# Optimization experiments

Measured on AMD Instinct MI355X. Metric: run time of the kernel, lower is better.

Reference implementation:

```python
import jax, jax.numpy as jnp
import numpy as np

H = 512       # hidden_dim == node_init_dim
N_MAX = 128   # max nodes (upper bound on ADD_NODE count)
L = 1024      # action sequence length (padded with -1)
NEG = -1e9    # mask value for invalid destination logits


def _gru(x, h, wih, whh, bih, bhh):
    # PyTorch nn.GRUCell math; gates packed as [r, z, n] along dim 0.
    gi = wih @ x + bih
    gh = whh @ h + bhh
    d = h.shape[0]
    r = jax.nn.sigmoid(gi[:d] + gh[:d])
    z = jax.nn.sigmoid(gi[d:2 * d] + gh[d:2 * d])
    n = jnp.tanh(gi[2 * d:] + r * gh[2 * d:])
    return (1.0 - z) * n + z * h


def _make_actions(rng):
    # Synthesize a grammatically valid DGMG teacher-forcing trace:
    # ADD_NODE=0, ADD_EDGE=1, CHOOSE_DEST=2, STOP_EDGE=3, STOP_NODE=4, pad=-1
    acts, ags = [], []
    cur = -1
    while len(acts) < L - 8 and cur < N_MAX - 1:
        acts.append(0); ags.append(0)
        cur += 1
        if cur > 0:
            for _ in range(int(rng.integers(1, 4))):
                if len(acts) >= L - 4:
                    break
                acts.append(1); ags.append(0)
                acts.append(2); ags.append(int(rng.integers(0, cur)))
            acts.append(3); ags.append(0)
    acts.append(4); ags.append(0)
    pad = L - len(acts)
    acts += [-1] * pad
    ags += [0] * pad
    return np.array(acts, np.int64), np.array(ags, np.int64)


def setup_inputs() -> dict:
    rng = np.random.default_rng(0)
    acts, ags = _make_actions(rng)
    key = jax.random.key(0)
    ks = jax.random.split(key, 12)
    s = 0.02
    p = lambda k, shape: jax.random.normal(k, shape, jnp.float32) * s
    return {
        "actions": jnp.asarray(acts),
        "args_seq": jnp.asarray(ags),
        "node_init": p(ks[0], (H,)),
        "w_nip": p(ks[1], (H, H)), "b_nip": jnp.zeros((H,), jnp.float32),
        "w_e1": p(ks[2], (H, 2 * H)), "b_e1": jnp.zeros((H,), jnp.float32),
        "w_e2": p(ks[3], (2, H)), "b_e2": jnp.zeros((2,), jnp.float32),
        "w_q": p(ks[4], (H, 2 * H)), "b_q": jnp.zeros((H,), jnp.float32),
        "w_k": p(ks[5], (H, H)), "b_k": jnp.zeros((H,), jnp.float32),
        "wih_n": p(ks[6], (3 * H, H)), "whh_n": p(ks[7], (3 * H, H)),
        "bih_n": jnp.zeros((3 * H,), jnp.float32), "bhh_n": jnp.zeros((3 * H,), jnp.float32),
        "wih_g": p(ks[8], (3 * H, H)), "whh_g": p(ks[9], (3 * H, H)),
        "bih_g": jnp.zeros((3 * H,), jnp.float32), "bhh_g": jnp.zeros((3 * H,), jnp.float32),
        "graph0": jnp.zeros((H,), jnp.float32),
    }


def reference(actions, args_seq, node_init, w_nip, b_nip, w_e1, b_e1, w_e2, b_e2,
              w_q, b_q, w_k, b_k, wih_n, whh_n, bih_n, bhh_n,
              wih_g, whh_g, bih_g, bhh_g, graph0):
    h0 = w_nip @ node_init + b_nip  # same fresh-node embedding for every ADD_NODE
    idx_range = jnp.arange(N_MAX)

    def edge_logits(g, curv):
        h = jax.nn.relu(w_e1 @ jnp.concatenate([g, curv]) + b_e1)
        return w_e2 @ h + b_e2  # (2,)

    def add_node(carry, arg):
        g, ne, cur, nll = carry
        cur2 = cur + 1
        ne2 = ne.at[cur2].set(h0)
        g2 = _gru(h0, g, wih_g, whh_g, bih_g, bhh_g)
        return (g2, ne2, cur2, nll)

    def add_edge(carry, arg):
        g, ne, cur, nll = carry
        nll2 = nll - jax.nn.log_softmax(edge_logits(g, ne[cur]))[0]
        return (g, ne, cur, nll2)

    def choose_dest(carry, arg):
        g, ne, cur, nll = carry
        curv = ne[cur]
        q = w_q @ jnp.concatenate([g, curv]) + b_q           # (H,)
        k = ne @ w_k.T + b_k                                  # (N_MAX, H)
        logits = jnp.where(idx_range < cur, k @ q, NEG)       # mask nodes >= cur
        nll2 = nll - jax.nn.log_softmax(logits)[arg]
        chosen = ne[arg]
        new_cur = _gru(chosen, curv, wih_n, whh_n, bih_n, bhh_n)
        ne2 = ne.at[cur].set(new_cur)
        g2 = _gru(new_cur, g, wih_g, whh_g, bih_g, bhh_g)
        return (g2, ne2, cur, nll2)

    def stop_edge(carry, arg):
        g, ne, cur, nll = carry
        nll2 = nll - jax.nn.log_softmax(edge_logits(g, ne[cur]))[1]
        return (g, ne, cur, nll2)

    def noop(carry, arg):
        return carry

    branches = [add_node, add_edge, choose_dest, stop_edge, noop]

    def step(carry, inp):
        a, arg = inp
        idx = jnp.where((a < 0) | (a >= 4), 4, a).astype(jnp.int32)
        return jax.lax.switch(idx, branches, carry, arg), None

    init = (graph0, jnp.zeros((N_MAX, H), graph0.dtype),
            jnp.int32(-1), jnp.zeros((), graph0.dtype))
    (g, ne, cur, nll), _ = jax.lax.scan(
        step, init, (actions.astype(jnp.int32), args_seq.astype(jnp.int32)))
    return nll
```

## Files before the change

### kernel.cpp

```cpp
#include <hip/hip_runtime.h>
#include <math.h>

#define NBLK 64
#define NTHR 576
#define LSEQ 1024

typedef unsigned int u32;
typedef unsigned short u16;
typedef unsigned long long u64;

__device__ __forceinline__ float bf2f(u16 u){ union{u32 i;float f;}v; v.i=(u32)u<<16; return v.f; }
__device__ __forceinline__ u16 f2bf(float f){ union{float f;u32 i;}v; v.f=f; u32 x=v.i;
  return (u16)((x + 0x7fffu + ((x>>16)&1u)) >> 16); }
__device__ __forceinline__ float u2f(u32 u){ union{u32 i;float f;}v; v.i=u; return v.f; }
__device__ __forceinline__ u32  f2u(float f){ union{float f;u32 i;}v; v.f=f; return v.i; }
__device__ __forceinline__ float sigm(float x){ return 1.f/(1.f+__expf(-x)); }

__device__ __forceinline__ u64 gld64(const u64* p){ return __hip_atomic_load(const_cast<u64*>(p), __ATOMIC_RELAXED, __HIP_MEMORY_SCOPE_AGENT); }
__device__ __forceinline__ void gst64(u64* p, u64 v){ __hip_atomic_store(p, v, __ATOMIC_RELAXED, __HIP_MEMORY_SCOPE_AGENT); }
__device__ __forceinline__ u64 pollt(const u64* p, u32 tag){
  u64 v; int n = 0;
  do { v = gld64(p); } while ((u32)(v>>32) != tag && ++n < (1<<20));
  return v;
}

__device__ __forceinline__ float wred(float a){
  a += __int_as_float(__builtin_amdgcn_update_dpp(0, __float_as_int(a), 0x111, 0xf, 0xf, true));
  a += __int_as_float(__builtin_amdgcn_update_dpp(0, __float_as_int(a), 0x112, 0xf, 0xf, true));
  a += __int_as_float(__builtin_amdgcn_update_dpp(0, __float_as_int(a), 0x114, 0xf, 0xf, true));
  a += __int_as_float(__builtin_amdgcn_update_dpp(0, __float_as_int(a), 0x118, 0xf, 0xf, true));
  a += __int_as_float(__builtin_amdgcn_update_dpp(0, __float_as_int(a), 0x142, 0xa, 0xf, true));
  a += __int_as_float(__builtin_amdgcn_update_dpp(0, __float_as_int(a), 0x143, 0xc, 0xf, true));
  return __int_as_float(__builtin_amdgcn_readlane(__float_as_int(a), 63));
}
__device__ __forceinline__ float wredsh(float a){
  #pragma unroll
  for (int off = 32; off; off >>= 1) a += __shfl_xor(a, off);
  return a;
}
__device__ __forceinline__ float wredmaxsh(float a){
  #pragma unroll
  for (int off = 32; off; off >>= 1) a = fmaxf(a, __shfl_xor(a, off));
  return a;
}

__device__ __forceinline__ float dot8p(uint4 w, float4 a, float4 b2){
  float s;
  s  = u2f(w.x<<16)*a.x  + u2f(w.x&0xffff0000u)*a.y;
  s += u2f(w.y<<16)*a.z  + u2f(w.y&0xffff0000u)*a.w;
  s += u2f(w.z<<16)*b2.x + u2f(w.z&0xffff0000u)*b2.y;
  s += u2f(w.w<<16)*b2.z + u2f(w.w&0xffff0000u)*b2.w;
  return s;
}
__device__ __forceinline__ float dot4f(float4 w, float4 x){
  return w.x*x.x + w.y*x.y + w.z*x.z + w.w*x.w;
}
__device__ __forceinline__ uint4 pk8(float4 a, float4 b2){
  uint4 r;
  r.x = (u32)f2bf(a.x)  | ((u32)f2bf(a.y)<<16);
  r.y = (u32)f2bf(a.z)  | ((u32)f2bf(a.w)<<16);
  r.z = (u32)f2bf(b2.x) | ((u32)f2bf(b2.y)<<16);
  r.w = (u32)f2bf(b2.z) | ((u32)f2bf(b2.w)<<16);
  return r;
}

#define SMEM_BYTES 150048

#define RUN_JOBS() do { \
  if (wv == 8){ \
    if (dBV && b == dBo1){ \
      u64 v_ = pollt(XS + dBSlot*64 + lane, dBTag); \
      float x0 = sA0 + bf2f((u16)(v_ & 0xffff)); \
      float x1 = sA1 + bf2f((u16)((v_>>16) & 0xffff)); \
      x0 = (lane < dBcur) ? x0 : -__builtin_inff(); \
      x1 = (lane + 64 < dBcur) ? x1 : -__builtin_inff(); \
      float m_ = wredmaxsh(fmaxf(x0, x1)); \
      float s_ = wredsh(__expf(x0 - m_) + __expf(x1 - m_)); \
      float la_ = (dBarg < 64) ? __shfl(x0, dBarg) : __shfl(x1, dBarg - 64); \
      if (lane == 0) nllw += (m_ + logf(s_)) - la_; \
    } \
    if (dAV && (b == dAo1 || b == dAo2)){ \
      const u64* P_ = XP + ((size_t)(dASlot*64 + lane))*64 + ((b == dAo2) ? 32 : 0); \
      float h0_ = 0.f, h1_ = 0.f; \
      for (int c_ = 0; c_ < 2; ++c_){ \
        u64 vv_[16]; int bad_; int nn_ = 0; \
        do { bad_ = 0; \
          _Pragma("unroll") for (int j_ = 0; j_ < 16; ++j_) vv_[j_] = gld64(P_ + c_*16 + j_); \
          _Pragma("unroll") for (int j_ = 0; j_ < 16; ++j_) bad_ |= ((u32)(vv_[j_]>>32) != dATag); \
        } while (bad_ && ++nn_ < (1<<20)); \
        _Pragma("unroll") for (int j_ = 0; j_ < 16; ++j_){ \
          h0_ += bf2f((u16)(vv_[j_] & 0xffff)); h1_ += bf2f((u16)((vv_[j_]>>16) & 0xffff)); } \
      } \
      if (b == dAo2) gst64(XS + dASlot*64 + lane, ((u64)dATag<<32) | (u32)f2bf(h0_) | ((u32)f2bf(h1_)<<16)); \
      else { sA0 = h0_; sA1 = h1_; } \
    } \
    if (aeV && b == aeOwn){ \
      u64 v_ = pollt(XE + aeSlot*64 + lane, aeTag); \
      float p0_ = wredsh(bf2f((u16)(v_ & 0xffff))); \
      float p1_ = wredsh(bf2f((u16)((v_>>16) & 0xffff))); \
      if (lane == 0){ \
        float l0_ = p0_ + be2_0, l1_ = p1_ + be2_1; \
        float m_ = fmaxf(l0_, l1_); \
        nllw += m_ + logf(__expf(l0_-m_) + __expf(l1_-m_)) - (aeSel ? l1_ : l0_); \
      } \
    } \
  } \
} while(0)

#define SHIFT_JOBS() do { \
  dBV = dAV; dBSlot = dASlot; dBo1 = dAo1; dBTag = dATag; dBcur = dAcur; dBarg = dAarg; \
  dAV = 0; aeV = 0; \
} while(0)

__global__ void __launch_bounds__(NTHR, 1)
dgmg_kernel(const int* __restrict__ actions, const int* __restrict__ argseq,
            const float* __restrict__ node_init, const float* __restrict__ w_nip, const float* __restrict__ b_nip,
            const float* __restrict__ w_e1, const float* __restrict__ b_e1,
            const float* __restrict__ w_e2, const float* __restrict__ b_e2,
            const float* __restrict__ w_q, const float* __restrict__ b_q,
            const float* __restrict__ w_k,
            const float* __restrict__ wih_n, const float* __restrict__ whh_n,
            const float* __restrict__ bih_n, const float* __restrict__ bhh_n,
            const float* __restrict__ wih_g, const float* __restrict__ whh_g,
            const float* __restrict__ bih_g, const float* __restrict__ bhh_g,
            const float* __restrict__ graph0,
            float* __restrict__ out, unsigned char* __restrict__ ws)
{
  extern __shared__ unsigned char smem[];
  u16* s_wihg = (u16*)smem;
  u16* s_whhg = s_wihg + 24*512;
  u16* s_wihn = s_whhg + 24*512;
  u16* s_whhn = s_wihn + 24*512;
  u16* s_we1  = s_whhn + 24*512;
  u16* s_wq   = s_we1 + 8*1024;
  float* s_g    = (float*)(s_wq + 8*1024);
  float* s_nc   = s_g + 512;
  float* s_curv = s_nc + 512;
  float* s_h0   = s_curv + 512;
  float* s_kloc = s_h0 + 512;
  float* s_bihg = s_kloc + 1024;
  float* s_bhhg = s_bihg + 24;
  float* s_bihn = s_bhhg + 24;
  float* s_bhhn = s_bihn + 24;
  float* s_be1  = s_bhhn + 24;
  float* s_bq   = s_be1 + 8;
  float* s_q8   = s_bq + 8;
  float* s_red  = s_q8 + 8;
  u16*   s_gin  = (u16*)(s_red + 16);

  const int b = blockIdx.x, tid = threadIdx.x;
  const int wv = tid >> 6, lane = tid & 63;
  const int d = b*8 + ((wv < 8) ? wv : 0);

  u64* Xng = (u64*)ws;
  u64* Xh  = Xng + 2048;
  u64* XE  = Xh + 512;
  u64* XP  = XE + 256;
  u64* XS  = XP + 16384;
  u64* XN  = XS + 256;

  if (tid < 24){
    int ld = tid/3, gt = tid%3;
    int row = gt*512 + b*8 + ld;
    s_bihg[tid] = bih_g[row]; s_bhhg[tid] = bhh_g[row];
    s_bihn[tid] = bih_n[row]; s_bhhn[tid] = bhh_n[row];
  }
  if (tid < 8){ s_be1[tid] = b_e1[b*8+tid]; s_bq[tid] = b_q[b*8+tid]; }

  for (int r = wv; r < 24; r += 9){
    int ld = r/3, gt = r%3;
    long grow = (long)(gt*512 + b*8 + ld) * 512;
    float4 a0, a1;
    a0 = *(const float4*)&wih_g[grow + lane*8]; a1 = *(const float4*)&wih_g[grow + lane*8 + 4];
    *(uint4*)&s_wihg[r*512 + lane*8] = pk8(a0, a1);
    a0 = *(const float4*)&whh_g[grow + lane*8]; a1 = *(const float4*)&whh_g[grow + lane*8 + 4];
    *(uint4*)&s_whhg[r*512 + lane*8] = pk8(a0, a1);
    a0 = *(const float4*)&wih_n[grow + lane*8]; a1 = *(const float4*)&wih_n[grow + lane*8 + 4];
    *(uint4*)&s_wihn[r*512 + lane*8] = pk8(a0, a1);
    a0 = *(const float4*)&whh_n[grow + lane*8]; a1 = *(const float4*)&whh_n[grow + lane*8 + 4];
    *(uint4*)&s_whhn[r*512 + lane*8] = pk8(a0, a1);
  }
  if (wv < 8){
    long grow = (long)(b*8 + wv) * 1024;
    #pragma unroll
    for (int h = 0; h < 2; ++h){
      float4 a0 = *(const float4*)&w_e1[grow + h*512 + lane*8];
      float4 a1 = *(const float4*)&w_e1[grow + h*512 + lane*8 + 4];
      *(uint4*)&s_we1[wv*1024 + h*512 + lane*8] = pk8(a0, a1);
      float4 q0 = *(const float4*)&w_q[grow + h*512 + lane*8];
      float4 q1 = *(const float4*)&w_q[grow + h*512 + lane*8 + 4];
      *(uint4*)&s_wq[wv*1024 + h*512 + lane*8] = pk8(q0, q1);
    }
  }
  float we2_0 = w_e2[d], we2_1 = w_e2[512+d];
  float be2_0 = b_e2[0], be2_1 = b_e2[1];
  float nllw = 0.f, sA0 = 0.f, sA1 = 0.f;

  int aeV=0, aeSlot=0, aeSel=0, aeOwn=0; u32 aeTag=0;
  int dAV=0, dASlot=0, dAo1=0, dAo2=0, dAcur=0, dAarg=0; u32 dATag=0;
  int dBV=0, dBSlot=0, dBo1=0, dBcur=0, dBarg=0; u32 dBTag=0;
  int ecnt=0, dcnt=0;

  if (tid < 512) s_g[tid] = node_init[tid];
  __syncthreads();
  float cbg_r=0,cbg_z=0,bg_ni=0,bg_nh=0, bh_gr=0,bh_gz=0;
  float bn_r=0,bn_z=0,bn_nh=0, fb_r=0,fb_z=0,fb_n=0, be1w=0,bqw=0;
  if (wv < 8){
    cbg_r = s_bihg[wv*3+0]+s_bhhg[wv*3+0];
    cbg_z = s_bihg[wv*3+1]+s_bhhg[wv*3+1];
    bg_ni = s_bihg[wv*3+2]; bg_nh = s_bhhg[wv*3+2];
    bh_gr = s_bhhg[wv*3+0]; bh_gz = s_bhhg[wv*3+1];
    bn_r = s_bhhn[wv*3+0]; bn_z = s_bhhn[wv*3+1]; bn_nh = s_bhhn[wv*3+2];
    fb_r = s_bihn[wv*3+0]; fb_z = s_bihn[wv*3+1]; fb_n = s_bihn[wv*3+2];
    be1w = s_be1[wv]; bqw = s_bq[wv];
    const float* wr = w_nip + (long)d*512;
    float4 wa = *(const float4*)&wr[lane*8], wb2 = *(const float4*)&wr[lane*8+4];
    float4 xa = *(float4*)&s_g[lane*8], xb = *(float4*)&s_g[lane*8+4];
    float h0d = wred(dot4f(wa,xa)+dot4f(wb2,xb)) + b_nip[d];
    if (lane == 0) gst64(&Xh[d], (1ull<<32) | f2u(h0d));
  }
  u32 ph = 2;

  float gi0r=0,gi0z=0,gi0n=0, ghn0r=0,ghn0z=0,ghn0n=0;
  int cur = -1, have_se = 0;
  bool first_an = true;

  for (int t = 0; t < LSEQ; ++t){
    int a = actions[t];
    if (a == 1) continue;
    if (a == 3){ have_se = 1; continue; }
    if (a < 0 || a >= 4) continue;

    int t1 = (t+1 < LSEQ) ? actions[t+1] : -1;
    int nxt = (t1 == 1);
    int i2 = (t+2 < LSEQ) ? t+2 : LSEQ-1;
    int chn = nxt ? argseq[i2] : 0;

    if (a == 0){
      int eslot = ecnt & 3;
      if (first_an){
        if (tid < 512){ u64 v = pollt(&Xh[tid], 1u); s_h0[tid] = u2f((u32)v); s_g[tid] = graph0[tid]; }
      } else {
        u32 gtag = ph-1; int gpar = gtag & 1;
        if (tid < 512){ u64 v = pollt(&Xng[(gpar*512+tid)*2+1], gtag); s_g[tid] = u2f((u32)v); }
      }
      __syncthreads();
      RUN_JOBS();
      if (wv < 8){
        float4 xg_a = *(float4*)&s_g[lane*8], xg_b = *(float4*)&s_g[lane*8+4];
        float4 xc_a = *(float4*)&s_curv[lane*8], xc_b = *(float4*)&s_curv[lane*8+4];
        const u32* Whg = (const u32*)s_whhg;
        if (first_an){
          float4 xh_a = *(float4*)&s_h0[lane*8], xh_b = *(float4*)&s_h0[lane*8+4];
          const u32* Wig = (const u32*)s_wihg; const u32* Wn = (const u32*)s_whhn;
          gi0r = wred(dot8p(*(const uint4*)&Wig[(wv*3+0)*256+lane*4], xh_a,xh_b)) + s_bihg[wv*3+0];
          gi0z = wred(dot8p(*(const uint4*)&Wig[(wv*3+1)*256+lane*4], xh_a,xh_b)) + s_bihg[wv*3+1];
          gi0n = wred(dot8p(*(const uint4*)&Wig[(wv*3+2)*256+lane*4], xh_a,xh_b)) + s_bihg[wv*3+2];
          ghn0r = wred(dot8p(*(const uint4*)&Wn[(wv*3+0)*256+lane*4], xh_a,xh_b)) + bn_r;
          ghn0z = wred(dot8p(*(const uint4*)&Wn[(wv*3+1)*256+lane*4], xh_a,xh_b)) + bn_z;
          ghn0n = wred(dot8p(*(const uint4*)&Wn[(wv*3+2)*256+lane*4], xh_a,xh_b)) + bn_nh;
        }
        {
          float ghr = wred(dot8p(*(const uint4*)&Whg[(wv*3+0)*256+lane*4], xg_a,xg_b)) + bh_gr;
          float ghz = wred(dot8p(*(const uint4*)&Whg[(wv*3+1)*256+lane*4], xg_a,xg_b)) + bh_gz;
          float ghn = wred(dot8p(*(const uint4*)&Whg[(wv*3+2)*256+lane*4], xg_a,xg_b)) + bg_nh;
          float r_ = sigm(gi0r + ghr), z_ = sigm(gi0z + ghz);
          float n_ = tanhf(gi0n + r_*ghn);
          if (lane == 0) gst64(&Xng[((ph&1)*512+d)*2+1], ((u64)ph<<32) | f2u((1.f-z_)*n_ + z_*s_g[d]));
        }
        float fr=0.f, fz=0.f, fn=0.f;
        if (cur >= 0){
          const u32* Win = (const u32*)s_wihn;
          fr = wred(dot8p(*(const uint4*)&Win[(wv*3+0)*256+lane*4], xc_a,xc_b)) + fb_r;
          fz = wred(dot8p(*(const uint4*)&Win[(wv*3+1)*256+lane*4], xc_a,xc_b)) + fb_z;
          fn = wred(dot8p(*(const uint4*)&Win[(wv*3+2)*256+lane*4], xc_a,xc_b)) + fb_n;
          float kv;
          {
            const float* wkr = w_k + (long)d*512;
            float4 ka = *(const float4*)&wkr[lane*8], kb2 = *(const float4*)&wkr[lane*8+4];
            kv = wred(dot4f(ka,xc_a)+dot4f(kb2,xc_b));
          }
          if (lane == 0){
            s_gin[cur*24+wv*3+0] = f2bf(fr); s_gin[cur*24+wv*3+1] = f2bf(fz); s_gin[cur*24+wv*3+2] = f2bf(fn);
            s_kloc[wv*128 + cur] = kv;
          }
        }
        if (nxt){
          float gr = (chn == cur && cur >= 0) ? fr : bf2f(s_gin[chn*24+wv*3+0]);
          float gz = (chn == cur && cur >= 0) ? fz : bf2f(s_gin[chn*24+wv*3+1]);
          float gn = (chn == cur && cur >= 0) ? fn : bf2f(s_gin[chn*24+wv*3+2]);
          float r2 = sigm(gr + ghn0r), z2 = sigm(gz + ghn0z);
          float n2 = tanhf(gn + r2*ghn0n);
          if (lane == 0) gst64(&Xng[((ph&1)*512+d)*2], ((u64)ph<<32) | f2u((1.f-z2)*n2 + z2*s_h0[d]));
        }
        if (have_se){
          const u32* Re = (const u32*)s_we1 + wv*512;
          float pe = dot8p(*(const uint4*)&Re[lane*4], xg_a,xg_b) + dot8p(*(const uint4*)&Re[256+lane*4], xc_a,xc_b);
          float hv = fmaxf(wred(pe) + be1w, 0.f);
          if (lane == 0){ s_red[wv*2+0] = hv*we2_0; s_red[wv*2+1] = hv*we2_1; }
        }
      }
      __syncthreads();
      if (have_se && tid == 0){
        float p0 = 0.f, p1 = 0.f;
        #pragma unroll
        for (int i = 0; i < 8; ++i){ p0 += s_red[i*2]; p1 += s_red[i*2+1]; }
        gst64(&XE[eslot*64 + b], ((u64)ph<<32) | (u32)f2bf(p0) | ((u32)f2bf(p1)<<16));
      }
      if (tid < 512) s_curv[tid] = s_h0[tid];
      SHIFT_JOBS();
      if (have_se){ aeV=1; aeSlot=eslot; aeSel=1; aeOwn=ecnt&63; aeTag=ph; ecnt++; }
      have_se = 0; first_an = false;
      cur += 1; ph += 1;
    }
    else {
      int arg = argseq[t];
      int eslot = ecnt & 3, dslot = dcnt & 1;
      {
        u32 gtag = ph-1; int gpar = gtag & 1;
        if (tid < 512){
          u64 v0, v1; int n = 0;
          const u64* p = &Xng[(gpar*512 + tid)*2];
          do { v0 = gld64(p); v1 = gld64(p+1); }
          while ((((u32)(v0>>32) != gtag) || ((u32)(v1>>32) != gtag)) && ++n < (1<<20));
          s_nc[tid] = u2f((u32)v0); s_g[tid] = u2f((u32)v1);
        }
      }
      __syncthreads();
      RUN_JOBS();
      if (wv < 8){
        float4 xn_a = *(float4*)&s_nc[lane*8], xn_b = *(float4*)&s_nc[lane*8+4];
        float4 xg_a = *(float4*)&s_g[lane*8],  xg_b = *(float4*)&s_g[lane*8+4];
        float4 xc_a = *(float4*)&s_curv[lane*8], xc_b = *(float4*)&s_curv[lane*8+4];
        const u32* Wn = (const u32*)s_whhn; const u32* Wig = (const u32*)s_wihg; const u32* Whg = (const u32*)s_whhg;
        {
          float pr = dot8p(*(const uint4*)&Wig[(wv*3+0)*256+lane*4], xn_a,xn_b)
                   + dot8p(*(const uint4*)&Whg[(wv*3+0)*256+lane*4], xg_a,xg_b);
          float pz = dot8p(*(const uint4*)&Wig[(wv*3+1)*256+lane*4], xn_a,xn_b)
                   + dot8p(*(const uint4*)&Whg[(wv*3+1)*256+lane*4], xg_a,xg_b);
          float r_ = sigm(wred(pr) + cbg_r);
          float z_ = sigm(wred(pz) + cbg_z);
          float gin_ = wred(dot8p(*(const uint4*)&Wig[(wv*3+2)*256+lane*4], xn_a,xn_b)) + bg_ni;
          float ghn_ = wred(dot8p(*(const uint4*)&Whg[(wv*3+2)*256+lane*4], xg_a,xg_b)) + bg_nh;
          float n_ = tanhf(gin_ + r_*ghn_);
          if (lane == 0) gst64(&Xng[((ph&1)*512+d)*2+1], ((u64)ph<<32) | f2u((1.f-z_)*n_ + z_*s_g[d]));
        }
        if (nxt){
          float ghr = wred(dot8p(*(const uint4*)&Wn[(wv*3+0)*256+lane*4], xn_a,xn_b)) + bn_r;
          float ghz = wred(dot8p(*(const uint4*)&Wn[(wv*3+1)*256+lane*4], xn_a,xn_b)) + bn_z;
          float ghn = wred(dot8p(*(const uint4*)&Wn[(wv*3+2)*256+lane*4], xn_a,xn_b)) + bn_nh;
          float gr = bf2f(s_gin[chn*24+wv*3+0]), gz = bf2f(s_gin[chn*24+wv*3+1]), gn = bf2f(s_gin[chn*24+wv*3+2]);
          float r_ = sigm(gr+ghr), z_ = sigm(gz+ghz);
          float n_ = tanhf(gn + r_*ghn);
          if (lane == 0) gst64(&Xng[((ph&1)*512+d)*2], ((u64)ph<<32) | f2u((1.f-z_)*n_ + z_*s_nc[d]));
        }
        {
          const u32* Rq = (const u32*)s_wq + wv*512;
          float pq = dot8p(*(const uint4*)&Rq[lane*4], xg_a,xg_b) + dot8p(*(const uint4*)&Rq[256+lane*4], xc_a,xc_b);
          float qd = wred(pq) + bqw;
          const u32* Re = (const u32*)s_we1 + wv*512;
          float pe = dot8p(*(const uint4*)&Re[lane*4], xg_a,xg_b) + dot8p(*(const uint4*)&Re[256+lane*4], xc_a,xc_b);
          float hv = fmaxf(wred(pe) + be1w, 0.f);
          if (lane == 0){ s_q8[wv] = qd; s_red[wv*2+0] = hv*we2_0; s_red[wv*2+1] = hv*we2_1; }
        }
      }
      __syncthreads();
      if (tid < 64){
        float pl0 = 0.f, pl1 = 0.f;
        #pragma unroll
        for (int k = 0; k < 8; ++k){
          pl0 += s_kloc[k*128 + tid]      * s_q8[k];
          pl1 += s_kloc[k*128 + tid + 64] * s_q8[k];
        }
        gst64(&XP[((size_t)(dslot*64 + tid))*64 + b],
              ((u64)ph<<32) | (u32)f2bf(pl0) | ((u32)f2bf(pl1)<<16));
      }
      if (tid == 64){
        float p0 = 0.f, p1 = 0.f;
        #pragma unroll
        for (int i = 0; i < 8; ++i){ p0 += s_red[i*2]; p1 += s_red[i*2+1]; }
        gst64(&XE[eslot*64 + b], ((u64)ph<<32) | (u32)f2bf(p0) | ((u32)f2bf(p1)<<16));
      }
      if (tid < 512) s_curv[tid] = s_nc[tid];
      SHIFT_JOBS();
      aeV=1; aeSlot=eslot; aeSel=0; aeOwn=ecnt&63; aeTag=ph; ecnt++;
      dAV=1; dASlot=dslot; dAo1=(2*dcnt)&63; dAo2=(2*dcnt+1)&63; dAcur=cur; dAarg=arg; dATag=ph;
      dcnt++;
      ph += 1;
    }
  }

  {
    int eslot = ecnt & 3;
    u32 gtag = ph-1; int gpar = gtag & 1;
    if (tid < 512){ u64 v = pollt(&Xng[(gpar*512+tid)*2+1], gtag); s_g[tid] = u2f((u32)v); }
    __syncthreads();
    RUN_JOBS();
    if (have_se && wv < 8){
      float4 xg_a = *(float4*)&s_g[lane*8], xg_b = *(float4*)&s_g[lane*8+4];
      float4 xc_a = *(float4*)&s_curv[lane*8], xc_b = *(float4*)&s_curv[lane*8+4];
      const u32* Re = (const u32*)s_we1 + wv*512;
      float pe = dot8p(*(const uint4*)&Re[lane*4], xg_a,xg_b) + dot8p(*(const uint4*)&Re[256+lane*4], xc_a,xc_b);
      float hv = fmaxf(wred(pe) + be1w, 0.f);
      if (lane == 0){ s_red[wv*2] = hv*we2_0; s_red[wv*2+1] = hv*we2_1; }
    }
    __syncthreads();
    if (have_se && tid == 0){
      float p0 = 0.f, p1 = 0.f;
      #pragma unroll
      for (int i = 0; i < 8; ++i){ p0 += s_red[i*2]; p1 += s_red[i*2+1]; }
      gst64(&XE[eslot*64 + b], ((u64)ph<<32) | (u32)f2bf(p0) | ((u32)f2bf(p1)<<16));
    }
    SHIFT_JOBS();
    RUN_JOBS();
    if (wv == 8){
      if (have_se && b == 0){
        u64 v = pollt(&XE[eslot*64 + lane], ph);
        float p0 = wredsh(bf2f((u16)(v & 0xffff)));
        float p1 = wredsh(bf2f((u16)((v>>16) & 0xffff)));
        if (lane == 0){
          float l0 = p0 + be2_0, l1 = p1 + be2_1;
          float m = fmaxf(l0, l1);
          nllw += m + logf(__expf(l0-m) + __expf(l1-m)) - l1;
        }
      }
      if (lane == 0) gst64(&XN[b], (0xFFFFull<<32) | f2u(nllw));
      if (b == 0){
        u64 v = pollt(&XN[lane], 0xFFFFu);
        float tot = wredsh(u2f((u32)v));
        if (lane == 0) out[0] = tot;
      }
    }
  }
}

extern "C" void kernel_launch(void* const* d_in, const int* in_sizes, int n_in,
                              void* d_out, int out_size, void* d_ws, size_t ws_size,
                              hipStream_t stream) {
  (void)in_sizes; (void)n_in; (void)out_size; (void)ws_size;
  hipMemsetAsync(d_ws, 0, 156160, stream);
  hipFuncSetAttribute((const void*)dgmg_kernel,
                      hipFuncAttributeMaxDynamicSharedMemorySize, SMEM_BYTES);
  dgmg_kernel<<<NBLK, NTHR, SMEM_BYTES, stream>>>(
      (const int*)d_in[0], (const int*)d_in[1],
      (const float*)d_in[2], (const float*)d_in[3], (const float*)d_in[4],
      (const float*)d_in[5], (const float*)d_in[6],
      (const float*)d_in[7], (const float*)d_in[8],
      (const float*)d_in[9], (const float*)d_in[10],
      (const float*)d_in[11],
      (const float*)d_in[13], (const float*)d_in[14],
      (const float*)d_in[15], (const float*)d_in[16],
      (const float*)d_in[17], (const float*)d_in[18],
      (const float*)d_in[19], (const float*)d_in[20],
      (const float*)d_in[21],
      (float*)d_out, (unsigned char*)d_ws);
}
```

Measured before the change: 1.108 ms.

## Replicate cross-block exchange buffers so block groups poll separate copies

Each producer block now writes its node/graph state values into 16 replicated copies of the global exchange buffers, and each group of four consumer blocks polls its own copy. The aim is to cut contention and cache-line ping-pong when all 64 blocks spin on the same addresses in the persistent-kernel handoff. In exchange, producers issue 16x more atomic stores on the critical path and the workspace memset grows.

```diff
diff --git a/kernel.cpp b/kernel.cpp
--- a/kernel.cpp
+++ b/kernel.cpp
@@ -4,6 +4,7 @@
 #define NBLK 64
 #define NTHR 576
 #define LSEQ 1024
+#define NCOPY 16
 
 typedef unsigned int u32;
 typedef unsigned short u16;
@@ -112,6 +113,13 @@
   dAV = 0; aeV = 0; \
 } while(0)
 
+#define FIRE_NG(par_, which_, val_) do { \
+  u64 atom_ = ((u64)ph<<32) | f2u(val_); \
+  _Pragma("unroll") \
+  for (int c_ = 0; c_ < NCOPY; ++c_) \
+    gst64(&Xng[((size_t)((par_)*NCOPY + c_)*512 + d)*2 + (which_)], atom_); \
+} while(0)
+
 __global__ void __launch_bounds__(NTHR, 1)
 dgmg_kernel(const int* __restrict__ actions, const int* __restrict__ argseq,
             const float* __restrict__ node_init, const float* __restrict__ w_nip, const float* __restrict__ b_nip,
@@ -151,10 +159,11 @@
   const int b = blockIdx.x, tid = threadIdx.x;
   const int wv = tid >> 6, lane = tid & 63;
   const int d = b*8 + ((wv < 8) ? wv : 0);
+  const int cpy = b >> 2;
 
   u64* Xng = (u64*)ws;
-  u64* Xh  = Xng + 2048;
-  u64* XE  = Xh + 512;
+  u64* Xh  = Xng + 32768;
+  u64* XE  = Xh + 8192;
   u64* XP  = XE + 256;
   u64* XS  = XP + 16384;
   u64* XN  = XS + 256;
@@ -217,7 +226,11 @@
     float4 wa = *(const float4*)&wr[lane*8], wb2 = *(const float4*)&wr[lane*8+4];
     float4 xa = *(float4*)&s_g[lane*8], xb = *(float4*)&s_g[lane*8+4];
     float h0d = wred(dot4f(wa,xa)+dot4f(wb2,xb)) + b_nip[d];
-    if (lane == 0) gst64(&Xh[d], (1ull<<32) | f2u(h0d));
+    if (lane == 0){
+      u64 atom = (1ull<<32) | f2u(h0d);
+      #pragma unroll
+      for (int c = 0; c < NCOPY; ++c) gst64(&Xh[(size_t)c*512 + d], atom);
+    }
   }
   u32 ph = 2;
 
@@ -239,10 +252,10 @@
     if (a == 0){
       int eslot = ecnt & 3;
       if (first_an){
-        if (tid < 512){ u64 v = pollt(&Xh[tid], 1u); s_h0[tid] = u2f((u32)v); s_g[tid] = graph0[tid]; }
+        if (tid < 512){ u64 v = pollt(&Xh[(size_t)cpy*512 + tid], 1u); s_h0[tid] = u2f((u32)v); s_g[tid] = graph0[tid]; }
       } else {
         u32 gtag = ph-1; int gpar = gtag & 1;
-        if (tid < 512){ u64 v = pollt(&Xng[(gpar*512+tid)*2+1], gtag); s_g[tid] = u2f((u32)v); }
+        if (tid < 512){ u64 v = pollt(&Xng[((size_t)(gpar*NCOPY+cpy)*512+tid)*2+1], gtag); s_g[tid] = u2f((u32)v); }
       }
       __syncthreads();
       RUN_JOBS();
@@ -266,7 +279,8 @@
           float ghn = wred(dot8p(*(const uint4*)&Whg[(wv*3+2)*256+lane*4], xg_a,xg_b)) + bg_nh;
           float r_ = sigm(gi0r + ghr), z_ = sigm(gi0z + ghz);
           float n_ = tanhf(gi0n + r_*ghn);
-          if (lane == 0) gst64(&Xng[((ph&1)*512+d)*2+1], ((u64)ph<<32) | f2u((1.f-z_)*n_ + z_*s_g[d]));
+          float gv = (1.f-z_)*n_ + z_*s_g[d];
+          if (lane == 0) FIRE_NG(ph&1, 1, gv);
         }
         float fr=0.f, fz=0.f, fn=0.f;
         if (cur >= 0){
@@ -291,7 +305,8 @@
           float gn = (chn == cur && cur >= 0) ? fn : bf2f(s_gin[chn*24+wv*3+2]);
           float r2 = sigm(gr + ghn0r), z2 = sigm(gz + ghn0z);
           float n2 = tanhf(gn + r2*ghn0n);
-          if (lane == 0) gst64(&Xng[((ph&1)*512+d)*2], ((u64)ph<<32) | f2u((1.f-z2)*n2 + z2*s_h0[d]));
+          float nv = (1.f-z2)*n2 + z2*s_h0[d];
+          if (lane == 0) FIRE_NG(ph&1, 0, nv);
         }
         if (have_se){
           const u32* Re = (const u32*)s_we1 + wv*512;
@@ -320,7 +335,7 @@
         u32 gtag = ph-1; int gpar = gtag & 1;
         if (tid < 512){
           u64 v0, v1; int n = 0;
-          const u64* p = &Xng[(gpar*512 + tid)*2];
+          const u64* p = &Xng[((size_t)(gpar*NCOPY+cpy)*512 + tid)*2];
           do { v0 = gld64(p); v1 = gld64(p+1); }
           while ((((u32)(v0>>32) != gtag) || ((u32)(v1>>32) != gtag)) && ++n < (1<<20));
           s_nc[tid] = u2f((u32)v0); s_g[tid] = u2f((u32)v1);
@@ -343,7 +358,8 @@
           float gin_ = wred(dot8p(*(const uint4*)&Wig[(wv*3+2)*256+lane*4], xn_a,xn_b)) + bg_ni;
           float ghn_ = wred(dot8p(*(const uint4*)&Whg[(wv*3+2)*256+lane*4], xg_a,xg_b)) + bg_nh;
           float n_ = tanhf(gin_ + r_*ghn_);
-          if (lane == 0) gst64(&Xng[((ph&1)*512+d)*2+1], ((u64)ph<<32) | f2u((1.f-z_)*n_ + z_*s_g[d]));
+          float gv = (1.f-z_)*n_ + z_*s_g[d];
+          if (lane == 0) FIRE_NG(ph&1, 1, gv);
         }
         if (nxt){
           float ghr = wred(dot8p(*(const uint4*)&Wn[(wv*3+0)*256+lane*4], xn_a,xn_b)) + bn_r;
@@ -352,7 +368,8 @@
           float gr = bf2f(s_gin[chn*24+wv*3+0]), gz = bf2f(s_gin[chn*24+wv*3+1]), gn = bf2f(s_gin[chn*24+wv*3+2]);
           float r_ = sigm(gr+ghr), z_ = sigm(gz+ghz);
           float n_ = tanhf(gn + r_*ghn);
-          if (lane == 0) gst64(&Xng[((ph&1)*512+d)*2], ((u64)ph<<32) | f2u((1.f-z_)*n_ + z_*s_nc[d]));
+          float nv = (1.f-z_)*n_ + z_*s_nc[d];
+          if (lane == 0) FIRE_NG(ph&1, 0, nv);
         }
         {
           const u32* Rq = (const u32*)s_wq + wv*512;
@@ -393,7 +410,7 @@
   {
     int eslot = ecnt & 3;
     u32 gtag = ph-1; int gpar = gtag & 1;
-    if (tid < 512){ u64 v = pollt(&Xng[(gpar*512+tid)*2+1], gtag); s_g[tid] = u2f((u32)v); }
+    if (tid < 512){ u64 v = pollt(&Xng[((size_t)(gpar*NCOPY+cpy)*512+tid)*2+1], gtag); s_g[tid] = u2f((u32)v); }
     __syncthreads();
     RUN_JOBS();
     if (have_se && wv < 8){
@@ -438,7 +455,7 @@
                               void* d_out, int out_size, void* d_ws, size_t ws_size,
                               hipStream_t stream) {
   (void)in_sizes; (void)n_in; (void)out_size; (void)ws_size;
-  hipMemsetAsync(d_ws, 0, 156160, stream);
+  hipMemsetAsync(d_ws, 0, 463360, stream);
   hipFuncSetAttribute((const void*)dgmg_kernel,
                       hipFuncAttributeMaxDynamicSharedMemorySize, SMEM_BYTES);
   dgmg_kernel<<<NBLK, NTHR, SMEM_BYTES, stream>>>(
```

Result: slower. 1.541 ms (+39.1%).
